# Kernel tuning notes

Hardware: AMD Instinct MI355X
Metric: run time of the kernel (lower is better)

The kernel has to match this reference:

```python
import jax, jax.numpy as jnp
import numpy as np

DEPTH_CHANNELS = 64
OUT_CHANNELS = 128
IN_CHANNELS = 256
BEV_W, BEV_H = 432, 496  # interpolate target size (height=432, width=496 in torch's (H,W) order)


def setup_inputs() -> dict:
    key = jax.random.key(0)
    k1, k2 = jax.random.split(key)
    B, H, W = 4, 32, 88
    feat_2d = jax.random.normal(k1, (B, IN_CHANNELS, H, W), dtype=jnp.float32)
    # conv1x1 weight: (out=64+128, in=256), bias (192,)
    Wc = jax.random.normal(k2, (DEPTH_CHANNELS + OUT_CHANNELS, IN_CHANNELS), dtype=jnp.float32) * 0.02
    bc = jnp.zeros((DEPTH_CHANNELS + OUT_CHANNELS,), dtype=jnp.float32)
    return {"feat_2d": feat_2d, "Wc": Wc, "bc": bc}


def reference(feat_2d, Wc, bc):
    # 1x1 conv == channel GEMM
    x = jnp.einsum('bihw,oi->bohw', feat_2d, Wc) + bc[None, :, None, None]
    depth = jax.nn.softmax(x[:, :DEPTH_CHANNELS], axis=1)      # (B,64,H,W)
    context = x[:, DEPTH_CHANNELS:]                            # (B,C,H,W)
    # mean_d(context[c] * depth[d]) == context[c] * mean_d(depth)  (algebraically identical)
    bev = context * jnp.mean(depth, axis=1, keepdims=True)     # (B,C,H,W)
    # bilinear upsample, half-pixel convention == torch align_corners=False (upsampling)
    B, C = bev.shape[0], bev.shape[1]
    bev = jax.image.resize(bev, (B, C, BEV_W, BEV_H), method='bilinear')
    return bev
```

## Files before the change

### kernel.cpp

```cpp
#include <hip/hip_runtime.h>


#define K_IN    256
#define C_CTX   128
#define C_DEPTH 64
#define H_IN    32
#define W_IN    88
#define POS     (H_IN * W_IN)
#define H_OUT   432
#define W_OUT   496
#define XG      (W_OUT / 4)
#define GPP     (XG * H_OUT)
#define NPLANE  (4 * C_CTX)
#define KC      64

typedef float f32x4 __attribute__((ext_vector_type(4)));

__global__ __launch_bounds__(256) void conv1x1_kernel(
    const float* __restrict__ feat, const float* __restrict__ Wc,
    const float* __restrict__ bc, float* __restrict__ ctx)
{
    __shared__ float As[KC * 64];
    __shared__ float Bs[KC * 64];

    const int t       = threadIdx.x;
    const int posbase = blockIdx.x * 64;
    const int cbase   = blockIdx.y * 64;
    const int b       = blockIdx.z;

    const int pg = t & 15;
    const int cg = t >> 4;

    const float* fb = feat + (size_t)b * K_IN * POS + posbase;
    const float* wb = Wc + (size_t)(C_DEPTH + cbase) * K_IN;

    float acc[4][4];
    #pragma unroll
    for (int i = 0; i < 4; ++i)
        #pragma unroll
        for (int j = 0; j < 4; ++j) acc[i][j] = 0.f;

    for (int kc = 0; kc < K_IN / KC; ++kc) {
        #pragma unroll
        for (int j = 0; j < 4; ++j) {
            int k  = (t >> 4) + 16 * j;
            int p4 = (t & 15) * 4;
            *(float4*)&As[k * 64 + p4] =
                *(const float4*)(fb + (size_t)(kc * KC + k) * POS + p4);
        }
        #pragma unroll
        for (int j = 0; j < 4; ++j) {
            int ch = t >> 2;
            int k  = (t & 3) * 4 + 16 * j;
            float4 w = *(const float4*)(wb + (size_t)ch * K_IN + kc * KC + k);
            Bs[(k + 0) * 64 + ch] = w.x;
            Bs[(k + 1) * 64 + ch] = w.y;
            Bs[(k + 2) * 64 + ch] = w.z;
            Bs[(k + 3) * 64 + ch] = w.w;
        }
        __syncthreads();

        #pragma unroll 8
        for (int k = 0; k < KC; ++k) {
            float4 a = *(const float4*)&As[k * 64 + pg * 4];
            float4 w = *(const float4*)&Bs[k * 64 + cg * 4];
            acc[0][0] = fmaf(a.x, w.x, acc[0][0]);
            acc[1][0] = fmaf(a.y, w.x, acc[1][0]);
            acc[2][0] = fmaf(a.z, w.x, acc[2][0]);
            acc[3][0] = fmaf(a.w, w.x, acc[3][0]);
            acc[0][1] = fmaf(a.x, w.y, acc[0][1]);
            acc[1][1] = fmaf(a.y, w.y, acc[1][1]);
            acc[2][1] = fmaf(a.z, w.y, acc[2][1]);
            acc[3][1] = fmaf(a.w, w.y, acc[3][1]);
            acc[0][2] = fmaf(a.x, w.z, acc[0][2]);
            acc[1][2] = fmaf(a.y, w.z, acc[1][2]);
            acc[2][2] = fmaf(a.z, w.z, acc[2][2]);
            acc[3][2] = fmaf(a.w, w.z, acc[3][2]);
            acc[0][3] = fmaf(a.x, w.w, acc[0][3]);
            acc[1][3] = fmaf(a.y, w.w, acc[1][3]);
            acc[2][3] = fmaf(a.z, w.w, acc[2][3]);
            acc[3][3] = fmaf(a.w, w.w, acc[3][3]);
        }
        __syncthreads();
    }

    const float s = 1.0f / 64.0f;
    #pragma unroll
    for (int j = 0; j < 4; ++j) {
        int ch = cbase + 4 * cg + j;
        float bb = bc[C_DEPTH + ch];
        float4 r;
        r.x = (acc[0][j] + bb) * s;
        r.y = (acc[1][j] + bb) * s;
        r.z = (acc[2][j] + bb) * s;
        r.w = (acc[3][j] + bb) * s;
        *(float4*)(ctx + (size_t)(b * C_CTX + ch) * POS + posbase + 4 * pg) = r;
    }
}

__global__ __launch_bounds__(256) void resize_kernel(
    const float* __restrict__ ctx, float* __restrict__ out)
{
    int g = blockIdx.x * blockDim.x + threadIdx.x;
    if (g >= GPP) return;
    int y  = g / XG;
    int xg = g - y * XG;
    int plane = blockIdx.y;

    const float* p = ctx + (size_t)plane * POS;

    const float SCY = 32.0f / 432.0f;
    const float SCX = 88.0f / 496.0f;

    float sy  = (y + 0.5f) * SCY - 0.5f;
    float fyf = floorf(sy);
    float wy  = sy - fyf;
    int y0  = (int)fyf;
    int y0c = max(y0, 0);
    int y1c = min(y0 + 1, H_IN - 1);
    const float* r0 = p + y0c * W_IN;
    const float* r1 = p + y1c * W_IN;

    float sx0 = (4 * xg + 0.5f) * SCX - 0.5f;
    int xb = (int)floorf(sx0);

    float ry[3];
    #pragma unroll
    for (int tp = 0; tp < 3; ++tp) {
        int xt = min(max(xb + tp, 0), W_IN - 1);
        float a = r0[xt];
        float b = r1[xt];
        ry[tp] = a + wy * (b - a);
    }

    float o[4];
    #pragma unroll
    for (int j = 0; j < 4; ++j) {
        float s  = (4 * xg + j + 0.5f) * SCX - 0.5f;
        float fs = floorf(s);
        float fx = s - fs;
        int tp = (int)fs - xb;
        o[j] = ry[tp] + fx * (ry[tp + 1] - ry[tp]);
    }

    size_t oidx = ((size_t)plane * H_OUT + y) * W_OUT + 4 * xg;
    f32x4 v = {o[0], o[1], o[2], o[3]};
    __builtin_nontemporal_store(v, (f32x4*)(out + oidx));
}

extern "C" void kernel_launch(void* const* d_in, const int* in_sizes, int n_in,
                              void* d_out, int out_size, void* d_ws, size_t ws_size,
                              hipStream_t stream) {
    const float* feat = (const float*)d_in[0];
    const float* Wc   = (const float*)d_in[1];
    const float* bc   = (const float*)d_in[2];
    float* out = (float*)d_out;
    float* ctx = (float*)d_ws;

    dim3 b1(256);
    dim3 g1(POS / 64, C_CTX / 64, 4);
    conv1x1_kernel<<<g1, b1, 0, stream>>>(feat, Wc, bc, ctx);

    dim3 b2(256);
    dim3 g2((GPP + 255) / 256, NPLANE);
    resize_kernel<<<g2, b2, 0, stream>>>(ctx, out);
}
```

Measured before the change: 451.7 us.

## Prefetch conv tiles in registers; batch four planes per resize thread with XCD remap

The conv kernel now loads the next K-chunk of activations and weights into registers while the current chunk is being computed, overlapping global loads with the FMA loop. The resize kernel has each thread handle four channel planes, reusing the coordinate and weight computations, and replaces the dynamically indexed ry array with selects. The resize grid is flattened to 1D, and block IDs are remapped so consecutive blocks spread in chunks across the 8 XCDs. These changes add register pressure and make each resize thread do more work, leaving fewer blocks.

Measured after the change: 458.0 us. About the same (+1.4%).

```diff
diff --git a/kernel.cpp b/kernel.cpp
--- a/kernel.cpp
+++ b/kernel.cpp
@@ -14,6 +14,12 @@
 #define NPLANE  (4 * C_CTX)
 #define KC      64
 
+#define PPT     4
+#define GY      (NPLANE / PPT)
+#define GX      ((GPP + 255) / 256)
+#define NBLK    (GX * GY)
+#define CHUNK   (NBLK / 8)
+
 typedef float f32x4 __attribute__((ext_vector_type(4)));
 
 __global__ __launch_bounds__(256) void conv1x1_kernel(
@@ -34,6 +40,18 @@
     const float* fb = feat + (size_t)b * K_IN * POS + posbase;
     const float* wb = Wc + (size_t)(C_DEPTH + cbase) * K_IN;
 
+    const int ka  = t >> 4;
+    const int pa  = (t & 15) * 4;
+    const int chB = t >> 2;
+    const int kB  = (t & 3) * 4;
+
+    float4 rA[4], rB[4];
+    #pragma unroll
+    for (int j = 0; j < 4; ++j) {
+        rA[j] = *(const float4*)(fb + (size_t)(ka + 16 * j) * POS + pa);
+        rB[j] = *(const float4*)(wb + (size_t)chB * K_IN + kB + 16 * j);
+    }
+
     float acc[4][4];
     #pragma unroll
     for (int i = 0; i < 4; ++i)
@@ -43,22 +61,23 @@
     for (int kc = 0; kc < K_IN / KC; ++kc) {
         #pragma unroll
         for (int j = 0; j < 4; ++j) {
-            int k  = (t >> 4) + 16 * j;
-            int p4 = (t & 15) * 4;
-            *(float4*)&As[k * 64 + p4] =
-                *(const float4*)(fb + (size_t)(kc * KC + k) * POS + p4);
-        }
-        #pragma unroll
-        for (int j = 0; j < 4; ++j) {
-            int ch = t >> 2;
-            int k  = (t & 3) * 4 + 16 * j;
-            float4 w = *(const float4*)(wb + (size_t)ch * K_IN + kc * KC + k);
-            Bs[(k + 0) * 64 + ch] = w.x;
-            Bs[(k + 1) * 64 + ch] = w.y;
-            Bs[(k + 2) * 64 + ch] = w.z;
-            Bs[(k + 3) * 64 + ch] = w.w;
+            *(float4*)&As[(ka + 16 * j) * 64 + pa] = rA[j];
+            Bs[(kB + 0 + 16 * j) * 64 + chB] = rB[j].x;
+            Bs[(kB + 1 + 16 * j) * 64 + chB] = rB[j].y;
+            Bs[(kB + 2 + 16 * j) * 64 + chB] = rB[j].z;
+            Bs[(kB + 3 + 16 * j) * 64 + chB] = rB[j].w;
         }
         __syncthreads();
+
+        if (kc < K_IN / KC - 1) {
+            #pragma unroll
+            for (int j = 0; j < 4; ++j) {
+                rA[j] = *(const float4*)(fb +
+                        (size_t)((kc + 1) * KC + ka + 16 * j) * POS + pa);
+                rB[j] = *(const float4*)(wb + (size_t)chB * K_IN +
+                        (kc + 1) * KC + kB + 16 * j);
+            }
+        }
 
         #pragma unroll 8
         for (int k = 0; k < KC; ++k) {
@@ -101,13 +120,16 @@
 __global__ __launch_bounds__(256) void resize_kernel(
     const float* __restrict__ ctx, float* __restrict__ out)
 {
-    int g = blockIdx.x * blockDim.x + threadIdx.x;
+    int bid = blockIdx.x;
+    int wg  = (bid & 7) * CHUNK + (bid >> 3);
+    int pg4 = wg / GX;
+    int gx  = wg - pg4 * GX;
+
+    int g = gx * 256 + threadIdx.x;
     if (g >= GPP) return;
     int y  = g / XG;
     int xg = g - y * XG;
-    int plane = blockIdx.y;
-
-    const float* p = ctx + (size_t)plane * POS;
+    int plane0 = pg4 * PPT;
 
     const float SCY = 32.0f / 432.0f;
     const float SCX = 88.0f / 496.0f;
@@ -118,34 +140,54 @@
     int y0  = (int)fyf;
     int y0c = max(y0, 0);
     int y1c = min(y0 + 1, H_IN - 1);
-    const float* r0 = p + y0c * W_IN;
-    const float* r1 = p + y1c * W_IN;
+    const int r0o = y0c * W_IN;
+    const int r1o = y1c * W_IN;
 
     float sx0 = (4 * xg + 0.5f) * SCX - 0.5f;
     int xb = (int)floorf(sx0);
 
-    float ry[3];
-    #pragma unroll
-    for (int tp = 0; tp < 3; ++tp) {
-        int xt = min(max(xb + tp, 0), W_IN - 1);
-        float a = r0[xt];
-        float b = r1[xt];
-        ry[tp] = a + wy * (b - a);
-    }
-
-    float o[4];
+    int xt[3];
+    #pragma unroll
+    for (int tp = 0; tp < 3; ++tp)
+        xt[tp] = min(max(xb + tp, 0), W_IN - 1);
+
+    float fx[4];
+    int   tj[4];
     #pragma unroll
     for (int j = 0; j < 4; ++j) {
         float s  = (4 * xg + j + 0.5f) * SCX - 0.5f;
         float fs = floorf(s);
-        float fx = s - fs;
-        int tp = (int)fs - xb;
-        o[j] = ry[tp] + fx * (ry[tp + 1] - ry[tp]);
-    }
-
-    size_t oidx = ((size_t)plane * H_OUT + y) * W_OUT + 4 * xg;
-    f32x4 v = {o[0], o[1], o[2], o[3]};
-    __builtin_nontemporal_store(v, (f32x4*)(out + oidx));
+        fx[j] = s - fs;
+        tj[j] = (int)fs - xb;
+    }
+
+    const float* p = ctx + (size_t)plane0 * POS;
+    size_t obase = ((size_t)plane0 * H_OUT + y) * W_OUT + 4 * xg;
+
+    #pragma unroll
+    for (int pp = 0; pp < PPT; ++pp) {
+        const float* r0 = p + (size_t)pp * POS + r0o;
+        const float* r1 = p + (size_t)pp * POS + r1o;
+        float ry0, ry1, ry2;
+        {
+            float a0 = r0[xt[0]], b0 = r1[xt[0]];
+            float a1 = r0[xt[1]], b1 = r1[xt[1]];
+            float a2 = r0[xt[2]], b2 = r1[xt[2]];
+            ry0 = a0 + wy * (b0 - a0);
+            ry1 = a1 + wy * (b1 - a1);
+            ry2 = a2 + wy * (b2 - a2);
+        }
+        float o[4];
+        #pragma unroll
+        for (int j = 0; j < 4; ++j) {
+            float lo = (tj[j] == 0) ? ry0 : ry1;
+            float hi = (tj[j] == 0) ? ry1 : ry2;
+            o[j] = lo + fx[j] * (hi - lo);
+        }
+        f32x4 v = {o[0], o[1], o[2], o[3]};
+        __builtin_nontemporal_store(v,
+            (f32x4*)(out + obase + (size_t)pp * (H_OUT * W_OUT)));
+    }
 }
 
 extern "C" void kernel_launch(void* const* d_in, const int* in_sizes, int n_in,
@@ -162,6 +204,6 @@
     conv1x1_kernel<<<g1, b1, 0, stream>>>(feat, Wc, bc, ctx);
 
     dim3 b2(256);
-    dim3 g2((GPP + 255) / 256, NPLANE);
+    dim3 g2(NBLK);
     resize_kernel<<<g2, b2, 0, stream>>>(ctx, out);
 }
```
